# Kernel tuning notes

Measured on AMD Instinct MI355X. Metric: run time of the kernel, lower is better.

## Reference

```python
import jax, jax.numpy as jnp
import numpy as np

N = 100_000          # nodes
E = 1_600_000        # directed edges (avg degree 16)
H = 128              # hidden_dim
OUT = 5              # output_dim (actions)
FOV = 11             # input_dim -> image side
LIN_IN = (FOV - 2) ** 2 * 3  # 243
LN_EPS = 1e-5


def _conv2d(x, w, b):
    # x: [N,3,h,w], w: [3,3,3,3] OIHW, VALID, stride 1
    y = jax.lax.conv_general_dilated(
        x, w, window_strides=(1, 1), padding='VALID',
        dimension_numbers=('NCHW', 'OIHW', 'NCHW'))
    return y + b[None, :, None, None]


def setup_inputs() -> dict:
    key = jax.random.key(0)
    ks = jax.random.split(key, 32)
    r = lambda i, shape, s=0.05: (jax.random.normal(ks[i], shape, jnp.float32) * s)
    inp = {
        'x': jax.random.normal(ks[0], (N, 3, FOV, FOV), jnp.float32),
        'edge_index': jax.random.randint(ks[1], (2, E), 0, N, jnp.int64)
                      if jax.config.jax_enable_x64 else
                      jax.random.randint(ks[1], (2, E), 0, N, jnp.int32),
        # CustomConv params
        'conv_w': r(2, (3, 3, 3, 3)), 'conv_b': r(3, (3,)),
        'conv_self_w': r(4, (3, 3, 3, 3)), 'conv_self_b': r(5, (3,)),
        'lin_w': r(6, (LIN_IN, H)), 'lin_b': r(7, (H,)),
        'lin_self_w': r(8, (LIN_IN, H)), 'lin_self_b': r(9, (H,)),
        # 3 SAGEConv layers: lin_l (aggregated, with bias), lin_r (root, no bias)
        'sage_lw': r(10, (3, H, H)), 'sage_lb': r(11, (3, H)),
        'sage_rw': r(12, (3, H, H)),
        # LayerNorms applied after layers 0,1,2
        'ln_g': jnp.ones((3, H), jnp.float32), 'ln_b': jnp.zeros((3, H), jnp.float32),
        # post_mp MLP (dropout is identity in eval)
        'mlp_w1': r(13, (H, H)), 'mlp_b1': r(14, (H,)),
        'mlp_w2': r(15, (H, OUT)), 'mlp_b2': r(16, (OUT,)),
    }
    return inp


def _layernorm(h, g, b):
    mu = jnp.mean(h, axis=-1, keepdims=True)
    var = jnp.var(h, axis=-1, keepdims=True)
    return (h - mu) * jax.lax.rsqrt(var + LN_EPS) * g + b


def reference(x, edge_index, conv_w, conv_b, conv_self_w, conv_self_b,
              lin_w, lin_b, lin_self_w, lin_self_b,
              sage_lw, sage_lb, sage_rw, ln_g, ln_b,
              mlp_w1, mlp_b1, mlp_w2, mlp_b2):
    src, dst = edge_index[0], edge_index[1]
    valid = (src != dst)  # remove_self_loops (CustomConv only)

    # ---- layer 0: CustomConv (add aggregation) ----
    self_x = jax.nn.relu(_conv2d(x, conv_self_w, conv_self_b).reshape(N, -1))
    self_x = self_x @ lin_self_w + lin_self_b              # [N,H]
    xn = jax.nn.relu(_conv2d(x, conv_w, conv_b).reshape(N, -1))
    xn = xn @ lin_w + lin_b                                # [N,H]
    msgs = xn[src] * valid[:, None].astype(xn.dtype)       # gather + mask self loops
    h = self_x + jax.ops.segment_sum(msgs, dst, num_segments=N)

    # SAGE mean-degree counts (all edges; SAGE does not remove self loops)
    cnt = jnp.maximum(
        jax.ops.segment_sum(jnp.ones((E,), h.dtype), dst, num_segments=N), 1.0)

    emb = h
    for i in range(4):
        if i > 0:
            j = i - 1
            agg = jax.ops.segment_sum(h[src], dst, num_segments=N) / cnt[:, None]
            h = agg @ sage_lw[j] + sage_lb[j] + h @ sage_rw[j]
        emb = h
        h = jax.nn.relu(h)            # dropout p=0.25 is identity in eval
        if i != 3:
            h = _layernorm(h, ln_g[i], ln_b[i])

    # task == 'node': no pooling
    logits = (h @ mlp_w1 + mlp_b1) @ mlp_w2 + mlp_b2
    return emb, jax.nn.log_softmax(logits, axis=1)
```

## Files before the change

### kernel.cpp

```cpp
#include <hip/hip_runtime.h>
#include <hip/hip_bf16.h>

typedef __hip_bfloat16 bf16;
typedef __attribute__((ext_vector_type(8))) short v8s;
typedef __attribute__((ext_vector_type(4))) float v4f;

#define N_NODES 100000
#define N_EDGES 1600000
#define LN_EPS 1e-5f

#define OFF_CONV_W      0
#define OFF_CONV_B      81
#define OFF_CONV_SW     84
#define OFF_CONV_SB     165
#define OFF_LIN_W       168
#define OFF_LIN_B       31272
#define OFF_LIN_SW      31400
#define OFF_LIN_SB      62504
#define OFF_SAGE_LW     62632
#define OFF_SAGE_LB     111784
#define OFF_SAGE_RW     112168
#define OFF_LN_G        161320
#define OFF_LN_B        161704
#define OFF_MLP_W1      162088
#define OFF_MLP_B1      178472
#define OFF_MLP_W2      178600
#define OFF_MLP_B2      179240
#define PARAM_TOTAL     179245

#define WTL_N 65536
#define WTS_N 98304
#define WTM_N 16384

#define CONV_NB 14

__device__ __forceinline__ unsigned short f2b(float f) {
    bf16 h = __float2bfloat16(f);
    return __builtin_bit_cast(unsigned short, h);
}
__device__ __forceinline__ float blo(unsigned u) { return __uint_as_float(u << 16); }
__device__ __forceinline__ float bhi(unsigned u) { return __uint_as_float(u & 0xffff0000u); }
__device__ __forceinline__ unsigned pack2(float lo, float hi) {
    return (unsigned)f2b(lo) | ((unsigned)f2b(hi) << 16);
}

struct Ptr17 { const void* p[17]; };

__global__ void detect_kernel(const unsigned short* __restrict__ xw,
                              const unsigned int* __restrict__ ew,
                              int* __restrict__ flags) {
    __shared__ int sawBigExp, sawHigh;
    if (threadIdx.x == 0) { sawBigExp = 0; sawHigh = 0; }
    __syncthreads();
    int localBig = 0, localHigh = 0;
    for (int i = threadIdx.x; i < 65536; i += 256) {
        unsigned e = (xw[i] >> 7) & 0xFF;
        if (e >= 0xF0) localBig = 1;
    }
    for (int i = threadIdx.x; i < 8192; i += 256) {
        if (ew[2 * i + 1] != 0) localHigh = 1;
    }
    if (localBig) atomicOr(&sawBigExp, 1);
    if (localHigh) atomicOr(&sawHigh, 1);
    __syncthreads();
    if (threadIdx.x == 0) { flags[0] = sawBigExp; flags[1] = sawHigh ? 0 : 1; }
}

__global__ void cvt_params_kernel(Ptr17 ptrs, const int* __restrict__ flags,
                                  float* __restrict__ dst) {
    int i = blockIdx.x * 256 + threadIdx.x;
    if (i >= PARAM_TOTAL) return;
    const int ksz[17] = {81,3,81,3,31104,128,31104,128,49152,384,49152,384,384,16384,128,640,5};
    int seg = 0, off = i;
    while (off >= ksz[seg]) { off -= ksz[seg]; ++seg; }
    float v;
    if (flags[0]) v = ((const float*)ptrs.p[seg])[off];
    else          v = __bfloat162float(((const bf16*)ptrs.p[seg])[off]);
    dst[i] = v;
}

__global__ void cvt2_kernel(const float* __restrict__ P,
                            unsigned short* __restrict__ wtl,
                            unsigned short* __restrict__ wts,
                            unsigned short* __restrict__ wtm) {
    int i = blockIdx.x * 256 + threadIdx.x;
    if (i < WTL_N) {
        int f = i >> 8, k = i & 255;
        float v = 0.f;
        if (k < 243) v = (f < 128) ? P[OFF_LIN_W + k * 128 + f]
                                   : P[OFF_LIN_SW + k * 128 + (f - 128)];
        wtl[i] = f2b(v);
    } else if (i < WTL_N + WTS_N) {
        int j = i - WTL_N; int l = j >> 15; int r = j & 32767; int f = r >> 8; int k = r & 255;
        float v = (k < 128) ? P[OFF_SAGE_LW + l * 16384 + k * 128 + f]
                            : P[OFF_SAGE_RW + l * 16384 + (k - 128) * 128 + f];
        wts[j] = f2b(v);
    } else if (i < WTL_N + WTS_N + WTM_N) {
        int j = i - WTL_N - WTS_N; int f = j >> 7, k = j & 127;
        wtm[j] = f2b(P[OFF_MLP_W1 + k * 128 + f]);
    }
}

__global__ __launch_bounds__(256) void conv_lin_kernel(
    const void* __restrict__ x, const float* __restrict__ P,
    const unsigned short* __restrict__ wtl, const int* __restrict__ flags,
    unsigned short* __restrict__ xnb, float* __restrict__ selfh)
{
    __shared__ float xs[CONV_NB][368];
    __shared__ unsigned short ysb[16][2][256];
    __shared__ float wconv[2][81];
    __shared__ float bconv[2][3];
    int tid = threadIdx.x;
    int n0 = blockIdx.x * CONV_NB;

    if (tid < 81) { wconv[0][tid] = P[OFF_CONV_W + tid]; wconv[1][tid] = P[OFF_CONV_SW + tid]; }
    else if (tid < 84) { int o = tid - 81; bconv[0][o] = P[OFF_CONV_B + o]; bconv[1][o] = P[OFF_CONV_SB + o]; }

    {
        unsigned int* z = (unsigned int*)ysb;
        #pragma unroll
        for (int i = tid; i < 16 * 2 * 128; i += 256) z[i] = 0;
    }
    if (flags[0]) {
        const float* xf = (const float*)x;
        for (int i = tid; i < CONV_NB * 363; i += 256) {
            int j = i / 363, q = i - j * 363;
            int node = n0 + j;
            xs[j][q] = (node < N_NODES) ? xf[(size_t)node * 363 + q] : 0.f;
        }
    } else {
        const unsigned short* xb = (const unsigned short*)x;
        for (int i = tid; i < CONV_NB * 363; i += 256) {
            int j = i / 363, q = i - j * 363;
            int node = n0 + j;
            xs[j][q] = (node < N_NODES) ? blo(xb[(size_t)node * 363 + q]) : 0.f;
        }
    }
    __syncthreads();

    if (tid < CONV_NB * 18) {
        int j = tid / 18, rem = tid - j * 18;
        int p = rem / 9, oi = rem - p * 9;
        float acc[27];
        #pragma unroll
        for (int o = 0; o < 3; o++) {
            float b = bconv[p][o];
            #pragma unroll
            for (int oj = 0; oj < 9; oj++) acc[o * 9 + oj] = b;
        }
        #pragma unroll
        for (int c = 0; c < 3; c++) {
            #pragma unroll
            for (int ki = 0; ki < 3; ki++) {
                float xr[11];
                const float* row = &xs[j][c * 121 + (oi + ki) * 11];
                #pragma unroll
                for (int t = 0; t < 11; t++) xr[t] = row[t];
                #pragma unroll
                for (int o = 0; o < 3; o++) {
                    int wb = o * 27 + c * 9 + ki * 3;
                    float w0 = wconv[p][wb], w1 = wconv[p][wb + 1], w2 = wconv[p][wb + 2];
                    #pragma unroll
                    for (int oj = 0; oj < 9; oj++)
                        acc[o * 9 + oj] += xr[oj] * w0 + xr[oj + 1] * w1 + xr[oj + 2] * w2;
                }
            }
        }
        #pragma unroll
        for (int o = 0; o < 3; o++)
            #pragma unroll
            for (int oj = 0; oj < 9; oj++)
                ysb[j][p][o * 81 + oi * 9 + oj] = f2b(fmaxf(acc[o * 9 + oj], 0.f));
    }
    __syncthreads();

    int wave = tid >> 6, lane = tid & 63, quad = lane >> 4, col = lane & 15;
    int p = wave >> 1;
    v4f acc[4];
    #pragma unroll
    for (int t = 0; t < 4; t++) { acc[t][0] = 0.f; acc[t][1] = 0.f; acc[t][2] = 0.f; acc[t][3] = 0.f; }
    for (int s = 0; s < 8; s++) {
        int kq = s * 32 + quad * 8;
        v8s a = *(const v8s*)&ysb[col][p][kq];
        #pragma unroll
        for (int t = 0; t < 4; t++) {
            int f = (wave * 4 + t) * 16 + col;
            v8s b = *(const v8s*)&wtl[(size_t)f * 256 + kq];
            acc[t] = __builtin_amdgcn_mfma_f32_16x16x32_bf16(a, b, acc[t], 0, 0, 0);
        }
    }
    #pragma unroll
    for (int t = 0; t < 4; t++) {
        int f = (wave * 4 + t) * 16 + col;
        #pragma unroll
        for (int r = 0; r < 4; r++) {
            int jj = quad * 4 + r;
            int node = n0 + jj;
            if (jj < CONV_NB && node < N_NODES) {
                float v = acc[t][r];
                if (p == 0) xnb[(size_t)node * 128 + f] = f2b(v + P[OFF_LIN_B + f]);
                else        selfh[(size_t)node * 128 + (f - 128)] = v + P[OFF_LIN_SB + (f - 128)];
            }
        }
    }
}

__device__ __forceinline__ int ld_edge(const int* __restrict__ ew, size_t elem, int isi64) {
    size_t idx = isi64 ? (elem * 2) : elem;
    return ew[idx];
}

__global__ void degree_kernel(const int* __restrict__ ew, const int* __restrict__ flags,
                              int* __restrict__ deg) {
    int e = blockIdx.x * blockDim.x + threadIdx.x;
    if (e < N_EDGES) {
        int d = ld_edge(ew, (size_t)N_EDGES + e, flags[1]);
        if ((unsigned)d < N_NODES) atomicAdd(&deg[d], 1);
    }
}

__global__ __launch_bounds__(1024) void scanA(const int* __restrict__ deg, int* __restrict__ rowptr,
                                              float* __restrict__ cntf, int* __restrict__ bsum) {
    __shared__ int s[1024];
    int tid = threadIdx.x;
    int i = blockIdx.x * 1024 + tid;
    int v = (i < N_NODES) ? deg[i] : 0;
    s[tid] = v;
    __syncthreads();
    for (int off = 1; off < 1024; off <<= 1) {
        int t = (tid >= off) ? s[tid - off] : 0;
        __syncthreads();
        s[tid] += t;
        __syncthreads();
    }
    if (i < N_NODES) {
        rowptr[i] = s[tid] - v;
        cntf[i] = (float)(v < 1 ? 1 : v);
    }
    if (tid == 1023) bsum[blockIdx.x] = s[1023];
}

__global__ void scanB(const int* __restrict__ bsum, int* __restrict__ boff, int nb, int* __restrict__ rowptr_end) {
    if (threadIdx.x == 0 && blockIdx.x == 0) {
        int run = 0;
        for (int i = 0; i < nb; i++) { boff[i] = run; run += bsum[i]; }
        *rowptr_end = run;
    }
}

__global__ __launch_bounds__(1024) void scanC(int* __restrict__ rowptr, const int* __restrict__ boff,
                                              int* __restrict__ cursor) {
    int i = blockIdx.x * 1024 + threadIdx.x;
    if (i < N_NODES) {
        int v = rowptr[i] + boff[blockIdx.x];
        rowptr[i] = v;
        cursor[i] = v;
    }
}

__global__ void fill_kernel(const int* __restrict__ ew, const int* __restrict__ flags,
                            int* __restrict__ cursor, int* __restrict__ csr) {
    int e = blockIdx.x * blockDim.x + threadIdx.x;
    if (e < N_EDGES) {
        int isi64 = flags[1];
        int s = ld_edge(ew, (size_t)e, isi64);
        int d = ld_edge(ew, (size_t)N_EDGES + e, isi64);
        if ((unsigned)d < N_NODES) {
            int p = atomicAdd(&cursor[d], 1);
            if ((unsigned)p < N_EDGES)
                csr[p] = ((unsigned)s < N_NODES) ? (s | ((s == d) ? (int)0x80000000 : 0)) : -1;
        }
    }
}

__global__ __launch_bounds__(256) void agg0ln_kernel(const unsigned short* __restrict__ xnb,
        const float* __restrict__ selfh, const int* __restrict__ rowptr, const int* __restrict__ csr,
        const float* __restrict__ lng, const float* __restrict__ lnb,
        unsigned short* __restrict__ zb) {
    int wave = threadIdx.x >> 6, lane = threadIdx.x & 63;
    int g = lane >> 4, c = lane & 15;
    int n = blockIdx.x * 4 + wave;
    int beg = rowptr[n], end = rowptr[n + 1];
    float a[8];
    #pragma unroll
    for (int i = 0; i < 8; i++) a[i] = 0.f;
    const uint4* x4 = (const uint4*)xnb;
    for (int b = beg; b < end; b += 64) {
        int bl = b + lane;
        int my = (bl < end) ? csr[bl] : -1;
        int nb = end - b; if (nb > 64) nb = 64;
        for (int i = 0; i < nb; i += 16) {
            int sv0 = __shfl(my, i + g, 64);
            int sv1 = __shfl(my, i + 4 + g, 64);
            int sv2 = __shfl(my, i + 8 + g, 64);
            int sv3 = __shfl(my, i + 12 + g, 64);
            bool va0 = ((unsigned)sv0 < N_NODES);
            bool va1 = ((unsigned)sv1 < N_NODES);
            bool va2 = ((unsigned)sv2 < N_NODES);
            bool va3 = ((unsigned)sv3 < N_NODES);
            uint4 v0 = x4[(size_t)(va0 ? sv0 : 0) * 16 + c];
            uint4 v1 = x4[(size_t)(va1 ? sv1 : 0) * 16 + c];
            uint4 v2 = x4[(size_t)(va2 ? sv2 : 0) * 16 + c];
            uint4 v3 = x4[(size_t)(va3 ? sv3 : 0) * 16 + c];
            if (va0) {
                a[0] += blo(v0.x); a[1] += bhi(v0.x);
                a[2] += blo(v0.y); a[3] += bhi(v0.y);
                a[4] += blo(v0.z); a[5] += bhi(v0.z);
                a[6] += blo(v0.w); a[7] += bhi(v0.w);
            }
            if (va1) {
                a[0] += blo(v1.x); a[1] += bhi(v1.x);
                a[2] += blo(v1.y); a[3] += bhi(v1.y);
                a[4] += blo(v1.z); a[5] += bhi(v1.z);
                a[6] += blo(v1.w); a[7] += bhi(v1.w);
            }
            if (va2) {
                a[0] += blo(v2.x); a[1] += bhi(v2.x);
                a[2] += blo(v2.y); a[3] += bhi(v2.y);
                a[4] += blo(v2.z); a[5] += bhi(v2.z);
                a[6] += blo(v2.w); a[7] += bhi(v2.w);
            }
            if (va3) {
                a[0] += blo(v3.x); a[1] += bhi(v3.x);
                a[2] += blo(v3.y); a[3] += bhi(v3.y);
                a[4] += blo(v3.z); a[5] += bhi(v3.z);
                a[6] += blo(v3.w); a[7] += bhi(v3.w);
            }
        }
    }
    #pragma unroll
    for (int i = 0; i < 8; i++) {
        a[i] += __shfl_xor(a[i], 16, 64);
        a[i] += __shfl_xor(a[i], 32, 64);
    }
    if (g == 0) {
        const float4* s4 = (const float4*)(selfh + (size_t)n * 128 + c * 8);
        float4 s0 = s4[0], s1 = s4[1];
        float v[8];
        v[0] = s0.x + a[0]; v[1] = s0.y + a[1]; v[2] = s0.z + a[2]; v[3] = s0.w + a[3];
        v[4] = s1.x + a[4]; v[5] = s1.y + a[5]; v[6] = s1.z + a[6]; v[7] = s1.w + a[7];
        float s = 0.f, sq = 0.f;
        #pragma unroll
        for (int i = 0; i < 8; i++) {
            v[i] = fmaxf(v[i], 0.f);
            s += v[i]; sq += v[i] * v[i];
        }
        #pragma unroll
        for (int m = 8; m >= 1; m >>= 1) {
            s  += __shfl_xor(s, m, 64);
            sq += __shfl_xor(sq, m, 64);
        }
        float mu = s * (1.f / 128.f);
        float var = sq * (1.f / 128.f) - mu * mu;
        float is = rsqrtf(var + LN_EPS);
        const float4* g4 = (const float4*)(lng + c * 8);
        const float4* b4 = (const float4*)(lnb + c * 8);
        float4 g0 = g4[0], g1 = g4[1], b0 = b4[0], b1 = b4[1];
        float z[8];
        z[0] = (v[0] - mu) * is * g0.x + b0.x; z[1] = (v[1] - mu) * is * g0.y + b0.y;
        z[2] = (v[2] - mu) * is * g0.z + b0.z; z[3] = (v[3] - mu) * is * g0.w + b0.w;
        z[4] = (v[4] - mu) * is * g1.x + b1.x; z[5] = (v[5] - mu) * is * g1.y + b1.y;
        z[6] = (v[6] - mu) * is * g1.z + b1.z; z[7] = (v[7] - mu) * is * g1.w + b1.w;
        uint4 o;
        o.x = pack2(z[0], z[1]); o.y = pack2(z[2], z[3]);
        o.z = pack2(z[4], z[5]); o.w = pack2(z[6], z[7]);
        ((uint4*)zb)[(size_t)n * 16 + c] = o;
    }
}

__global__ __launch_bounds__(256) void aggm_kernel(const unsigned short* __restrict__ zb,
        const int* __restrict__ rowptr, const int* __restrict__ csr,
        const float* __restrict__ cntf, unsigned short* __restrict__ aggb) {
    int wave = threadIdx.x >> 6, lane = threadIdx.x & 63;
    int g = lane >> 4, c = lane & 15;
    int n = blockIdx.x * 4 + wave;
    int beg = rowptr[n], end = rowptr[n + 1];
    float a[8];
    #pragma unroll
    for (int i = 0; i < 8; i++) a[i] = 0.f;
    const uint4* z4 = (const uint4*)zb;
    for (int b = beg; b < end; b += 64) {
        int bl = b + lane;
        int my = (bl < end) ? csr[bl] : -1;
        int nb = end - b; if (nb > 64) nb = 64;
        for (int i = 0; i < nb; i += 16) {
            int sv0 = __shfl(my, i + g, 64) & 0x7fffffff;
            int sv1 = __shfl(my, i + 4 + g, 64) & 0x7fffffff;
            int sv2 = __shfl(my, i + 8 + g, 64) & 0x7fffffff;
            int sv3 = __shfl(my, i + 12 + g, 64) & 0x7fffffff;
            bool va0 = (sv0 < N_NODES);
            bool va1 = (sv1 < N_NODES);
            bool va2 = (sv2 < N_NODES);
            bool va3 = (sv3 < N_NODES);
            uint4 v0 = z4[(size_t)(va0 ? sv0 : 0) * 16 + c];
            uint4 v1 = z4[(size_t)(va1 ? sv1 : 0) * 16 + c];
            uint4 v2 = z4[(size_t)(va2 ? sv2 : 0) * 16 + c];
            uint4 v3 = z4[(size_t)(va3 ? sv3 : 0) * 16 + c];
            if (va0) {
                a[0] += blo(v0.x); a[1] += bhi(v0.x);
                a[2] += blo(v0.y); a[3] += bhi(v0.y);
                a[4] += blo(v0.z); a[5] += bhi(v0.z);
                a[6] += blo(v0.w); a[7] += bhi(v0.w);
            }
            if (va1) {
                a[0] += blo(v1.x); a[1] += bhi(v1.x);
                a[2] += blo(v1.y); a[3] += bhi(v1.y);
                a[4] += blo(v1.z); a[5] += bhi(v1.z);
                a[6] += blo(v1.w); a[7] += bhi(v1.w);
            }
            if (va2) {
                a[0] += blo(v2.x); a[1] += bhi(v2.x);
                a[2] += blo(v2.y); a[3] += bhi(v2.y);
                a[4] += blo(v2.z); a[5] += bhi(v2.z);
                a[6] += blo(v2.w); a[7] += bhi(v2.w);
            }
            if (va3) {
                a[0] += blo(v3.x); a[1] += bhi(v3.x);
                a[2] += blo(v3.y); a[3] += bhi(v3.y);
                a[4] += blo(v3.z); a[5] += bhi(v3.z);
                a[6] += blo(v3.w); a[7] += bhi(v3.w);
            }
        }
    }
    #pragma unroll
    for (int i = 0; i < 8; i++) {
        a[i] += __shfl_xor(a[i], 16, 64);
        a[i] += __shfl_xor(a[i], 32, 64);
    }
    if (g == 0) {
        float inv = 1.f / cntf[n];
        uint4 o;
        o.x = pack2(a[0] * inv, a[1] * inv); o.y = pack2(a[2] * inv, a[3] * inv);
        o.z = pack2(a[4] * inv, a[5] * inv); o.w = pack2(a[6] * inv, a[7] * inv);
        ((uint4*)aggb)[(size_t)n * 16 + c] = o;
    }
}

__global__ __launch_bounds__(256) void sageln_kernel(const unsigned short* __restrict__ aggb,
        unsigned short* __restrict__ zb, const unsigned short* __restrict__ wts,
        const float* __restrict__ lb, const float* __restrict__ lng, const float* __restrict__ lnb,
        int last, float* __restrict__ hout) {
    __shared__ float hb[16][128];
    int tid = threadIdx.x;
    int n0 = blockIdx.x * 16;
    int wave = tid >> 6, lane = tid & 63, quad = lane >> 4, col = lane & 15;
    int nodeA = n0 + col;

    v4f acc[2];
    #pragma unroll
    for (int t = 0; t < 2; t++) { acc[t][0] = 0.f; acc[t][1] = 0.f; acc[t][2] = 0.f; acc[t][3] = 0.f; }
    #pragma unroll
    for (int s = 0; s < 8; s++) {
        int kq = s * 32 + quad * 8;
        const unsigned short* abase = (s < 4) ? (aggb + (size_t)nodeA * 128 + kq)
                                              : (zb + (size_t)nodeA * 128 + (kq - 128));
        v8s a = *(const v8s*)abase;
        #pragma unroll
        for (int t = 0; t < 2; t++) {
            int f = (wave * 2 + t) * 16 + col;
            v8s b = *(const v8s*)&wts[(size_t)f * 256 + kq];
            acc[t] = __builtin_amdgcn_mfma_f32_16x16x32_bf16(a, b, acc[t], 0, 0, 0);
        }
    }
    #pragma unroll
    for (int t = 0; t < 2; t++) {
        int f = (wave * 2 + t) * 16 + col;
        float bias = lb[f];
        #pragma unroll
        for (int r = 0; r < 4; r++)
            hb[quad * 4 + r][f] = acc[t][r] + bias;
    }
    __syncthreads();

    #pragma unroll
    for (int jj = 0; jj < 4; jj++) {
        int j = wave * 4 + jj;
        int node = n0 + j;
        float v0 = hb[j][2 * lane], v1 = hb[j][2 * lane + 1];
        if (last) {
            float2 w; w.x = v0; w.y = v1;
            ((float2*)hout)[(size_t)node * 64 + lane] = w;
        } else {
            float r0 = fmaxf(v0, 0.f), r1 = fmaxf(v1, 0.f);
            float s = r0 + r1, sq = r0 * r0 + r1 * r1;
            #pragma unroll
            for (int m = 32; m >= 1; m >>= 1) {
                s  += __shfl_xor(s, m, 64);
                sq += __shfl_xor(sq, m, 64);
            }
            float mu = s * (1.f / 128.f);
            float var = sq * (1.f / 128.f) - mu * mu;
            float inv = rsqrtf(var + LN_EPS);
            float z0 = (r0 - mu) * inv * lng[2 * lane]     + lnb[2 * lane];
            float z1 = (r1 - mu) * inv * lng[2 * lane + 1] + lnb[2 * lane + 1];
            ((unsigned int*)zb)[(size_t)node * 64 + lane] = pack2(z0, z1);
        }
    }
}

__global__ __launch_bounds__(256) void mlp_kernel(const float* __restrict__ h,
        const unsigned short* __restrict__ wtm, const float* __restrict__ P,
        const int* __restrict__ flags, void* __restrict__ out) {
    __shared__ unsigned short rb[16][128];
    __shared__ float mb[16][128];
    __shared__ float lg[16][5];
    int tid = threadIdx.x;
    int n0 = blockIdx.x * 16;
    int isf = flags[0];

    const float2* h2 = (const float2*)h;
    for (int i = tid; i < 16 * 64; i += 256) {
        int j = i >> 6, q = i & 63;
        float2 v = h2[(size_t)(n0 + j) * 64 + q];
        size_t oi = (size_t)(n0 + j) * 128 + 2 * q;
        if (isf) { ((float*)out)[oi] = v.x; ((float*)out)[oi + 1] = v.y; }
        else ((unsigned int*)out)[oi >> 1] = pack2(v.x, v.y);
        rb[j][2 * q]     = f2b(fmaxf(v.x, 0.f));
        rb[j][2 * q + 1] = f2b(fmaxf(v.y, 0.f));
    }
    __syncthreads();

    int wave = tid >> 6, lane = tid & 63, quad = lane >> 4, col = lane & 15;
    v4f acc[2];
    #pragma unroll
    for (int t = 0; t < 2; t++) { acc[t][0] = 0.f; acc[t][1] = 0.f; acc[t][2] = 0.f; acc[t][3] = 0.f; }
    #pragma unroll
    for (int s = 0; s < 4; s++) {
        int kq = s * 32 + quad * 8;
        v8s a = *(const v8s*)&rb[col][kq];
        #pragma unroll
        for (int t = 0; t < 2; t++) {
            int f = (wave * 2 + t) * 16 + col;
            v8s b = *(const v8s*)&wtm[(size_t)f * 128 + kq];
            acc[t] = __builtin_amdgcn_mfma_f32_16x16x32_bf16(a, b, acc[t], 0, 0, 0);
        }
    }
    #pragma unroll
    for (int t = 0; t < 2; t++) {
        int f = (wave * 2 + t) * 16 + col;
        float bias = P[OFF_MLP_B1 + f];
        #pragma unroll
        for (int r = 0; r < 4; r++)
            mb[quad * 4 + r][f] = acc[t][r] + bias;
    }
    __syncthreads();

    if (tid < 80) {
        int j = tid / 5, o = tid - (tid / 5) * 5;
        float a = P[OFF_MLP_B2 + o];
        for (int k = 0; k < 128; k++) a += mb[j][k] * P[OFF_MLP_W2 + k * 5 + o];
        lg[j][o] = a;
    }
    __syncthreads();
    if (tid < 16) {
        int j = tid;
        float mx = lg[j][0];
        #pragma unroll
        for (int o = 1; o < 5; o++) mx = fmaxf(mx, lg[j][o]);
        float se = 0.f;
        #pragma unroll
        for (int o = 0; o < 5; o++) se += expf(lg[j][o] - mx);
        float lse = mx + logf(se);
        size_t base = (size_t)N_NODES * 128 + (size_t)(n0 + j) * 5;
        #pragma unroll
        for (int o = 0; o < 5; o++) {
            float v = lg[j][o] - lse;
            if (isf) ((float*)out)[base + o] = v;
            else     ((bf16*)out)[base + o] = __float2bfloat16(v);
        }
    }
}

extern "C" void kernel_launch(void* const* d_in, const int* in_sizes, int n_in,
                              void* d_out, int out_size, void* d_ws, size_t ws_size,
                              hipStream_t stream) {
    const void* x  = d_in[0];
    const int*  ew = (const int*)d_in[1];

    Ptr17 ptrs;
    for (int i = 0; i < 17; i++) ptrs.p[i] = d_in[2 + i];

    char* w = (char*)d_ws;
    auto carve = [&](size_t bytes) { char* r = w; w += (bytes + 255) & ~(size_t)255; return r; };
    float*          bufS  = (float*)carve((size_t)N_NODES * 128 * 4);
    unsigned short* xnb   = (unsigned short*)carve((size_t)N_NODES * 128 * 2);
    unsigned short* zb    = (unsigned short*)carve((size_t)N_NODES * 128 * 2);
    unsigned short* aggb  = (unsigned short*)carve((size_t)N_NODES * 128 * 2);
    float*          pf32  = (float*)carve((size_t)PARAM_TOTAL * 4);
    unsigned short* wtl   = (unsigned short*)carve((size_t)WTL_N * 2);
    unsigned short* wts   = (unsigned short*)carve((size_t)WTS_N * 2);
    unsigned short* wtm   = (unsigned short*)carve((size_t)WTM_N * 2);
    int*   deg    = (int*)carve((size_t)N_NODES * 4);
    int*   rowptr = (int*)carve((size_t)(N_NODES + 64) * 4);
    int*   cursor = (int*)carve((size_t)N_NODES * 4);
    float* cntf   = (float*)carve((size_t)N_NODES * 4);
    int*   bsum   = (int*)carve(512);
    int*   boff   = (int*)carve(512);
    int*   flags  = (int*)carve(256);
    int*   csr    = (int*)carve((size_t)N_EDGES * 4);

    const int SCAN_BLOCKS = (N_NODES + 1023) / 1024;
    const int CONV_BLOCKS = (N_NODES + CONV_NB - 1) / CONV_NB;

    detect_kernel<<<1, 256, 0, stream>>>((const unsigned short*)x, (const unsigned int*)ew, flags);
    cvt_params_kernel<<<(PARAM_TOTAL + 255) / 256, 256, 0, stream>>>(ptrs, flags, pf32);
    cvt2_kernel<<<(WTL_N + WTS_N + WTM_N + 255) / 256, 256, 0, stream>>>(pf32, wtl, wts, wtm);

    hipMemsetAsync(deg, 0, (size_t)N_NODES * 4, stream);

    conv_lin_kernel<<<CONV_BLOCKS, 256, 0, stream>>>(x, pf32, wtl, flags, xnb, bufS);

    degree_kernel<<<(N_EDGES + 255) / 256, 256, 0, stream>>>(ew, flags, deg);
    scanA<<<SCAN_BLOCKS, 1024, 0, stream>>>(deg, rowptr, cntf, bsum);
    scanB<<<1, 1, 0, stream>>>(bsum, boff, SCAN_BLOCKS, rowptr + N_NODES);
    scanC<<<SCAN_BLOCKS, 1024, 0, stream>>>(rowptr, boff, cursor);
    fill_kernel<<<(N_EDGES + 255) / 256, 256, 0, stream>>>(ew, flags, cursor, csr);

    agg0ln_kernel<<<N_NODES / 4, 256, 0, stream>>>(xnb, bufS, rowptr, csr,
        pf32 + OFF_LN_G, pf32 + OFF_LN_B, zb);

    for (int l = 0; l < 3; l++) {
        aggm_kernel<<<N_NODES / 4, 256, 0, stream>>>(zb, rowptr, csr, cntf, aggb);
        sageln_kernel<<<N_NODES / 16, 256, 0, stream>>>(aggb, zb, wts + (size_t)l * 32768,
            pf32 + OFF_SAGE_LB + l * 128,
            pf32 + OFF_LN_G + (l + 1) * 128, pf32 + OFF_LN_B + (l + 1) * 128,
            (l == 2) ? 1 : 0, bufS);
    }

    mlp_kernel<<<N_NODES / 16, 256, 0, stream>>>(bufS, wtm, pf32, flags, d_out);
}
```

Before: 1.215 ms.

## Process 16 nodes per conv block with 320 threads and bf16 staging

The conv+linear kernel now handles 16 nodes per block instead of 14, so every MFMA row is used and the tail checks disappear. It launches 320 threads so all 288 conv work items run at once. The input tile is staged in shared memory as bf16, with 16-byte vector copies when the input is already bf16. Only the padding columns of the conv output buffer are zeroed. In exchange it drops the node bounds checks, relying on N being divisible by 16, and rounds fp32 inputs to bf16 before the convolution.

```diff
diff --git a/kernel.cpp b/kernel.cpp
--- a/kernel.cpp
+++ b/kernel.cpp
@@ -31,8 +31,6 @@
 #define WTL_N 65536
 #define WTS_N 98304
 #define WTM_N 16384
-
-#define CONV_NB 14
 
 __device__ __forceinline__ unsigned short f2b(float f) {
     bf16 h = __float2bfloat16(f);
@@ -101,50 +99,43 @@
     }
 }
 
-__global__ __launch_bounds__(256) void conv_lin_kernel(
+__global__ __launch_bounds__(320) void conv_lin_kernel(
     const void* __restrict__ x, const float* __restrict__ P,
     const unsigned short* __restrict__ wtl, const int* __restrict__ flags,
     unsigned short* __restrict__ xnb, float* __restrict__ selfh)
 {
-    __shared__ float xs[CONV_NB][368];
+    __shared__ unsigned short xs[5808];
     __shared__ unsigned short ysb[16][2][256];
-    __shared__ float wconv[2][81];
-    __shared__ float bconv[2][3];
+    __shared__ float wc[2][81];
+    __shared__ float bc[2][3];
     int tid = threadIdx.x;
-    int n0 = blockIdx.x * CONV_NB;
-
-    if (tid < 81) { wconv[0][tid] = P[OFF_CONV_W + tid]; wconv[1][tid] = P[OFF_CONV_SW + tid]; }
-    else if (tid < 84) { int o = tid - 81; bconv[0][o] = P[OFF_CONV_B + o]; bconv[1][o] = P[OFF_CONV_SB + o]; }
-
-    {
-        unsigned int* z = (unsigned int*)ysb;
-        #pragma unroll
-        for (int i = tid; i < 16 * 2 * 128; i += 256) z[i] = 0;
-    }
+    int n0 = blockIdx.x * 16;
+
+    if (tid < 81) { wc[0][tid] = P[OFF_CONV_W + tid]; wc[1][tid] = P[OFF_CONV_SW + tid]; }
+    else if (tid < 84) { int o = tid - 81; bc[0][o] = P[OFF_CONV_B + o]; bc[1][o] = P[OFF_CONV_SB + o]; }
+
+    for (int i = tid; i < 416; i += 320) {
+        int j = i / 26, r2 = i % 26, p = r2 / 13, k = 243 + (r2 % 13);
+        ysb[j][p][k] = 0;
+    }
+
     if (flags[0]) {
-        const float* xf = (const float*)x;
-        for (int i = tid; i < CONV_NB * 363; i += 256) {
-            int j = i / 363, q = i - j * 363;
-            int node = n0 + j;
-            xs[j][q] = (node < N_NODES) ? xf[(size_t)node * 363 + q] : 0.f;
-        }
+        const float* xf = (const float*)x + (size_t)n0 * 363;
+        for (int i = tid; i < 5808; i += 320) xs[i] = f2b(xf[i]);
     } else {
-        const unsigned short* xb = (const unsigned short*)x;
-        for (int i = tid; i < CONV_NB * 363; i += 256) {
-            int j = i / 363, q = i - j * 363;
-            int node = n0 + j;
-            xs[j][q] = (node < N_NODES) ? blo(xb[(size_t)node * 363 + q]) : 0.f;
-        }
-    }
-    __syncthreads();
-
-    if (tid < CONV_NB * 18) {
-        int j = tid / 18, rem = tid - j * 18;
-        int p = rem / 9, oi = rem - p * 9;
+        const uint4* xsrc = (const uint4*)((const unsigned short*)x + (size_t)n0 * 363);
+        uint4* xd = (uint4*)xs;
+        for (int i = tid; i < 726; i += 320) xd[i] = xsrc[i];
+    }
+    __syncthreads();
+
+    if (tid < 288) {
+        int j = tid / 18, rem = tid % 18;
+        int p = rem / 9, oi = rem % 9;
         float acc[27];
         #pragma unroll
         for (int o = 0; o < 3; o++) {
-            float b = bconv[p][o];
+            float b = bc[p][o];
             #pragma unroll
             for (int oj = 0; oj < 9; oj++) acc[o * 9 + oj] = b;
         }
@@ -153,13 +144,13 @@
             #pragma unroll
             for (int ki = 0; ki < 3; ki++) {
                 float xr[11];
-                const float* row = &xs[j][c * 121 + (oi + ki) * 11];
+                const unsigned short* row = &xs[j * 363 + c * 121 + (oi + ki) * 11];
                 #pragma unroll
-                for (int t = 0; t < 11; t++) xr[t] = row[t];
+                for (int t = 0; t < 11; t++) xr[t] = blo(row[t]);
                 #pragma unroll
                 for (int o = 0; o < 3; o++) {
                     int wb = o * 27 + c * 9 + ki * 3;
-                    float w0 = wconv[p][wb], w1 = wconv[p][wb + 1], w2 = wconv[p][wb + 2];
+                    float w0 = wc[p][wb], w1 = wc[p][wb + 1], w2 = wc[p][wb + 2];
                     #pragma unroll
                     for (int oj = 0; oj < 9; oj++)
                         acc[o * 9 + oj] += xr[oj] * w0 + xr[oj + 1] * w1 + xr[oj + 2] * w2;
@@ -175,28 +166,27 @@
     __syncthreads();
 
     int wave = tid >> 6, lane = tid & 63, quad = lane >> 4, col = lane & 15;
-    int p = wave >> 1;
-    v4f acc[4];
-    #pragma unroll
-    for (int t = 0; t < 4; t++) { acc[t][0] = 0.f; acc[t][1] = 0.f; acc[t][2] = 0.f; acc[t][3] = 0.f; }
-    for (int s = 0; s < 8; s++) {
-        int kq = s * 32 + quad * 8;
-        v8s a = *(const v8s*)&ysb[col][p][kq];
+    if (wave < 4) {
+        int p = wave >> 1;
+        v4f acc[4];
+        #pragma unroll
+        for (int t = 0; t < 4; t++) { acc[t][0] = 0.f; acc[t][1] = 0.f; acc[t][2] = 0.f; acc[t][3] = 0.f; }
+        for (int s = 0; s < 8; s++) {
+            int kq = s * 32 + quad * 8;
+            v8s a = *(const v8s*)&ysb[col][p][kq];
+            #pragma unroll
+            for (int t = 0; t < 4; t++) {
+                int f = (wave * 4 + t) * 16 + col;
+                v8s b = *(const v8s*)&wtl[(size_t)f * 256 + kq];
+                acc[t] = __builtin_amdgcn_mfma_f32_16x16x32_bf16(a, b, acc[t], 0, 0, 0);
+            }
+        }
         #pragma unroll
         for (int t = 0; t < 4; t++) {
             int f = (wave * 4 + t) * 16 + col;
-            v8s b = *(const v8s*)&wtl[(size_t)f * 256 + kq];
-            acc[t] = __builtin_amdgcn_mfma_f32_16x16x32_bf16(a, b, acc[t], 0, 0, 0);
-        }
-    }
-    #pragma unroll
-    for (int t = 0; t < 4; t++) {
-        int f = (wave * 4 + t) * 16 + col;
-        #pragma unroll
-        for (int r = 0; r < 4; r++) {
-            int jj = quad * 4 + r;
-            int node = n0 + jj;
-            if (jj < CONV_NB && node < N_NODES) {
+            #pragma unroll
+            for (int r = 0; r < 4; r++) {
+                int node = n0 + quad * 4 + r;
                 float v = acc[t][r];
                 if (p == 0) xnb[(size_t)node * 128 + f] = f2b(v + P[OFF_LIN_B + f]);
                 else        selfh[(size_t)node * 128 + (f - 128)] = v + P[OFF_LIN_SB + (f - 128)];
@@ -600,7 +590,6 @@
     int*   csr    = (int*)carve((size_t)N_EDGES * 4);
 
     const int SCAN_BLOCKS = (N_NODES + 1023) / 1024;
-    const int CONV_BLOCKS = (N_NODES + CONV_NB - 1) / CONV_NB;
 
     detect_kernel<<<1, 256, 0, stream>>>((const unsigned short*)x, (const unsigned int*)ew, flags);
     cvt_params_kernel<<<(PARAM_TOTAL + 255) / 256, 256, 0, stream>>>(ptrs, flags, pf32);
@@ -608,7 +597,7 @@
 
     hipMemsetAsync(deg, 0, (size_t)N_NODES * 4, stream);
 
-    conv_lin_kernel<<<CONV_BLOCKS, 256, 0, stream>>>(x, pf32, wtl, flags, xnb, bufS);
+    conv_lin_kernel<<<N_NODES / 16, 320, 0, stream>>>(x, pf32, wtl, flags, xnb, bufS);
 
     degree_kernel<<<(N_EDGES + 255) / 256, 256, 0, stream>>>(ew, flags, deg);
     scanA<<<SCAN_BLOCKS, 1024, 0, stream>>>(deg, rowptr, cntf, bsum);
```

Result: faster. 1.150 ms (-5.3%).
